# Performance work log

Hardware: AMD Instinct MI355X
Metric: run time of the kernel (lower is better)

The kernel has to match this reference:

```python
import jax, jax.numpy as jnp
import numpy as np

VOLRADIUS = 256.0
DT = 1.0 / VOLRADIUS  # self.dt = dt / volradius with dt=1.0
N_STEPS = 64
B, H, W, K, M = 1, 256, 256, 64, 16


def setup_inputs() -> dict:
    rng = np.random.default_rng(0)
    # orthographic-ish ray bundle looking down +z through the primitive cloud
    ys, xs = np.meshgrid(np.linspace(-1., 1., H, dtype=np.float32),
                         np.linspace(-1., 1., W, dtype=np.float32), indexing='ij')
    raypos = np.broadcast_to(np.stack([xs, ys, np.full_like(xs, -0.125)], -1)[None],
                             (B, H, W, 3)).astype(np.float32).copy()
    raydir = np.zeros((B, H, W, 3), np.float32); raydir[..., 2] = 1.0
    tmin = np.zeros((B, H, W), np.float32)
    tminmax = np.stack([tmin, tmin + N_STEPS * DT], -1).astype(np.float32)
    # primpos is in WORLD units (module divides by volradius)
    primpos = rng.uniform(-0.1 * VOLRADIUS, 0.1 * VOLRADIUS, (B, K, 3)).astype(np.float32)
    q, _ = np.linalg.qr(rng.normal(size=(B, K, 3, 3)))
    primrot = q.astype(np.float32)
    primscale = rng.uniform(8., 16., (B, K, 3)).astype(np.float32)  # inverse half-extent
    primrgba = rng.uniform(0., 1., (B, K, 4, M, M, M)).astype(np.float32)
    return {
        'raypos': jnp.asarray(raypos), 'raydir': jnp.asarray(raydir),
        'tminmax': jnp.asarray(tminmax), 'primpos': jnp.asarray(primpos),
        'primrot': jnp.asarray(primrot), 'primscale': jnproundtrip(primscale) if False else jnp.asarray(primscale),
        'primrgba': jnp.asarray(primrgba),
    }


def _trilinear_sum(template, pos, primpos, primrot, primscale):
    # template [K,4,M,M,M]; pos [R,3]; returns summed rgba over primitives [R,4]
    Mv = template.shape[-1]
    kidx = jnp.arange(template.shape[0])[None, :]                      # [1,K]
    rel = pos[:, None, :] - primpos[None, :, :]                        # [R,K,3]
    # local = primscale * (primrot^T @ rel), inside prim iff |local| < 1
    local = jnp.einsum('kij,rki->rkj', primrot, rel) * primscale[None]  # [R,K,3]
    inside = jnp.all(jnp.abs(local) < 1.0, axis=-1)                    # [R,K]
    g = jnp.clip((local + 1.0) * 0.5 * (Mv - 1), 0.0, Mv - 1 - 1e-5)    # voxel coords (x,y,z)
    i0 = jnp.clip(jnp.floor(g).astype(jnp.int32), 0, Mv - 2)
    f = g - i0.astype(g.dtype)
    x0, y0, z0 = i0[..., 0], i0[..., 1], i0[..., 2]
    fx, fy, fz = f[..., 0], f[..., 1], f[..., 2]
    c = jnp.zeros(local.shape[:2] + (4,), template.dtype)
    for dz, wz in ((0, 1 - fz), (1, fz)):
        for dy, wy in ((0, 1 - fy), (1, fy)):
            for dx, wx in ((0, 1 - fx), (1, fx)):
                corner = template[kidx, :, z0 + dz, y0 + dy, x0 + dx]  # [R,K,4]
                c = c + corner * (wz * wy * wx)[..., None]
    c = c * inside[..., None]
    return c.sum(axis=1)                                               # [R,4]


def _march(raypos, raydir, tminmax, primpos, primrot, primscale, template):
    Hh, Ww, _ = raypos.shape
    R = Hh * Ww
    o = raypos.reshape(R, 3)
    d = raydir.reshape(R, 3)
    tmm = tminmax.reshape(R, 2)
    tmin, tmax = tmm[:, 0], tmm[:, 1]

    def step(carry, i):
        rgb, alpha = carry
        t = tmin + (i.astype(jnp.float32) + 0.5) * DT
        valid = t < tmax
        pos = o + t[:, None] * d
        s = _trilinear_sum(template, pos, primpos, primrot, primscale)  # [R,4]
        # MVP front-to-back saturating alpha compositing (early-term equivalent)
        contrib = jnp.minimum(1.0, alpha + s[:, 3] * DT) - alpha
        contrib = jnp.where(valid, contrib, 0.0)
        rgb = rgb + s[:, :3] * contrib[:, None]
        alpha = alpha + contrib
        return (rgb, alpha), None

    init = (jnp.zeros((R, 3), jnp.float32), jnp.zeros((R,), jnp.float32))
    (rgb, alpha), _ = jax.lax.scan(jax.checkpoint(step), init, jnp.arange(N_STEPS))
    return jnp.concatenate([rgb, alpha[:, None]], -1).reshape(Hh, Ww, 4)


def reference(raypos, raydir, tminmax, primpos, primrot, primscale, primrgba):
    primpos_n = primpos / VOLRADIUS  # module normalizes primpos by volume radius
    rayrgba = jax.vmap(_march)(raypos, raydir, tminmax, primpos_n, primrot, primscale, primrgba)
    rayrgba = jnp.transpose(rayrgba, (0, 3, 1, 2))  # [B,4,H,W]
    rayrgb = rayrgba[:, :3]
    rayalpha = rayrgba[:, 3:4]
    return rayrgb, rayalpha, rayrgba
```

## Files before the change

kernel.cpp:

```cpp
#include <hip/hip_runtime.h>
#include <hip/hip_fp16.h>

#define Rtot 65536
#define Wimg 256
#define Kp 64
#define NSTEPS 64
#define DTc (1.0f/256.0f)
#define INV_VOLR (1.0f/256.0f)
#define NITEMS 16384

#define PD_OFF    0u
#define TB_OFF    4096u
#define FLAG_OFF  20480u
#define TT_OFF    65536u
#define SBUF_OFF  8388608u
#define WS_NEED   (SBUF_OFF + (size_t)NITEMS*256*8)

__device__ __forceinline__ unsigned int pack2(float a, float b) {
  __half2 h = __floats2half2_rn(a, b);
  return *(unsigned int*)&h;
}

__global__ __launch_bounds__(256) void setup_kernel(
    const float* __restrict__ raypos, const float* __restrict__ raydir,
    const float* __restrict__ tminmax, const float* __restrict__ primpos,
    const float* __restrict__ primrot, const float* __restrict__ primscale,
    const float* __restrict__ tmpl,
    float* __restrict__ tb, uint4* __restrict__ tth, float* __restrict__ pd) {
  int bid = blockIdx.x, tid = threadIdx.x;
  if (bid < 256) {
    __shared__ float smn[4][7], smx[4][7];
    int w = (bid & 15)*16 + (tid & 15);
    int h = (bid >> 4)*16 + (tid >> 4);
    int r = h*Wimg + w;
    float v[7];
    v[0] = raypos[r*3+0]; v[1] = raypos[r*3+1]; v[2] = raypos[r*3+2];
    v[3] = raydir[r*3+0]; v[4] = raydir[r*3+1]; v[5] = raydir[r*3+2];
    v[6] = tminmax[r*2+0];
    float mn[7], mx[7];
#pragma unroll
    for (int i = 0; i < 7; ++i) { mn[i] = v[i]; mx[i] = v[i]; }
#pragma unroll
    for (int m = 1; m < 64; m <<= 1) {
#pragma unroll
      for (int i = 0; i < 7; ++i) {
        mn[i] = fminf(mn[i], __shfl_xor(mn[i], m));
        mx[i] = fmaxf(mx[i], __shfl_xor(mx[i], m));
      }
    }
    int wv = tid >> 6;
    if ((tid & 63) == 0) {
#pragma unroll
      for (int i = 0; i < 7; ++i) { smn[wv][i] = mn[i]; smx[wv][i] = mx[i]; }
    }
    __syncthreads();
    if (tid == 0) {
#pragma unroll
      for (int i = 0; i < 7; ++i) {
        tb[bid*16 + i]     = fminf(fminf(smn[0][i], smn[1][i]), fminf(smn[2][i], smn[3][i]));
        tb[bid*16 + 8 + i] = fmaxf(fmaxf(smx[0][i], smx[1][i]), fmaxf(smx[2][i], smx[3][i]));
      }
    }
  } else if (bid < 320) {
    int k = bid - 256;
    const float* b0 = tmpl + (((size_t)k) << 14);
    uint4* o = tth + (k << 12);
    for (int v = tid; v < 4096; v += 256) {
      int x = v & 15;
      int xn = (x < 15) ? v + 1 : v;
      uint4 q;
      q.x = pack2(b0[v],       b0[4096+v]);
      q.y = pack2(b0[8192+v],  b0[12288+v]);
      q.z = pack2(b0[xn],      b0[4096+xn]);
      q.w = pack2(b0[8192+xn], b0[12288+xn]);
      o[v] = q;
    }
  } else {
    int k = tid;
    if (k < Kp) {
      float sc0 = primscale[k*3+0], sc1 = primscale[k*3+1], sc2 = primscale[k*3+2];
      float* o = pd + (k << 4);
      o[0] = primpos[k*3+0] * INV_VOLR;
      o[1] = primpos[k*3+1] * INV_VOLR;
      o[2] = primpos[k*3+2] * INV_VOLR;
      o[3] = 0.0f; o[4] = 0.0f; o[5] = 0.0f;
#pragma unroll
      for (int i = 0; i < 3; ++i) {
        o[6+i*3+0] = primrot[k*9+i*3+0]*sc0;
        o[6+i*3+1] = primrot[k*9+i*3+1]*sc1;
        o[6+i*3+2] = primrot[k*9+i*3+2]*sc2;
      }
      o[15] = 0.0f;
    }
  }
}

__device__ __forceinline__ void prim_setup(const float* __restrict__ p,
    float px, float py, float pz, bool& inside, const uint4*& addr,
    float& wx0, float& wfx, float& w00, float& w01, float& w10, float& w11,
    const uint4* __restrict__ tth, int k) {
  float relx = px - p[0], rely = py - p[1], relz = pz - p[2];
  float lx = relx*p[6] + rely*p[9]  + relz*p[12];
  float ly = relx*p[7] + rely*p[10] + relz*p[13];
  float lz = relx*p[8] + rely*p[11] + relz*p[14];
  inside = fabsf(lx) < 1.0f && fabsf(ly) < 1.0f && fabsf(lz) < 1.0f;
  float gx = fminf(fmaxf((lx + 1.0f)*7.5f, 0.0f), 14.99999f);
  float gy = fminf(fmaxf((ly + 1.0f)*7.5f, 0.0f), 14.99999f);
  float gz = fminf(fmaxf((lz + 1.0f)*7.5f, 0.0f), 14.99999f);
  int ix = (int)gx, iy = (int)gy, iz = (int)gz;
  ix = ix > 14 ? 14 : ix; iy = iy > 14 ? 14 : iy; iz = iz > 14 ? 14 : iz;
  float fx = gx - (float)ix, fy = gy - (float)iy, fz = gz - (float)iz;
  float m = inside ? 1.0f : 0.0f;
  wx0 = 1.0f - fx; wfx = fx;
  float wy0 = 1.0f - fy, wz0 = 1.0f - fz;
  w00 = wz0*wy0*m; w01 = wz0*fy*m; w10 = fz*wy0*m; w11 = fz*fy*m;
  addr = tth + ((size_t)k << 12) + iz*256 + iy*16 + ix;
}

#define ACCQ(q, wv, wx0, wfx) { \
  float2 p01 = __half22float2(*(const __half2*)&q.x); \
  float2 p23 = __half22float2(*(const __half2*)&q.y); \
  float2 n01 = __half22float2(*(const __half2*)&q.z); \
  float2 n23 = __half22float2(*(const __half2*)&q.w); \
  float wa = (wv)*(wx0), wb = (wv)*(wfx); \
  c0 = fmaf(p01.x, wa, fmaf(n01.x, wb, c0)); \
  c1 = fmaf(p01.y, wa, fmaf(n01.y, wb, c1)); \
  c2 = fmaf(p23.x, wa, fmaf(n23.x, wb, c2)); \
  c3 = fmaf(p23.y, wa, fmaf(n23.y, wb, c3)); }

__global__ __launch_bounds__(256) void shade_kernel(
    const float* __restrict__ raypos, const float* __restrict__ raydir,
    const float* __restrict__ tminmax, const float* __restrict__ pd,
    const float* __restrict__ tb, const uint4* __restrict__ tth,
    uint2* __restrict__ sbuf, unsigned char* __restrict__ flags) {
  __shared__ int s_list[Kp];
  __shared__ int s_cnt;
  int item = blockIdx.x;
  int tile = item >> 6, step = item & 63;
  int tid = threadIdx.x;
  if (tid < 64) {
    const float* t0 = tb + tile*16;
    float cst = ((float)step + 0.5f)*DTc;
    float tl = t0[6] + cst, th = t0[14] + cst;
    const float* p = pd + (tid << 4);
    float rlo[3], rhi[3];
#pragma unroll
    for (int a = 0; a < 3; ++a) {
      float ol = t0[a], oh = t0[8+a], dl = t0[3+a], dh = t0[11+a];
      float p1 = tl*dl, p2 = tl*dh, p3 = th*dl, p4 = th*dh;
      float lo = ol + fminf(fminf(p1, p2), fminf(p3, p4));
      float hi = oh + fmaxf(fmaxf(p1, p2), fmaxf(p3, p4));
      rlo[a] = lo - p[a];
      rhi[a] = hi - p[a];
    }
    bool pass = true;
#pragma unroll
    for (int j = 0; j < 3; ++j) {
      float llo = 0.f, lhi = 0.f;
#pragma unroll
      for (int a = 0; a < 3; ++a) {
        float rsc = p[6+a*3+j];
        float q1 = rlo[a]*rsc, q2 = rhi[a]*rsc;
        llo += fminf(q1, q2);
        lhi += fmaxf(q1, q2);
      }
      pass = pass && (llo < 1.0f) && (lhi > -1.0f);
    }
    unsigned long long mask = __ballot(pass);
    if (tid == 0) s_cnt = (int)__popcll(mask);
    if (pass) {
      int pos = (int)__popcll(mask & ((1ull << tid) - 1ull));
      s_list[pos] = tid;
    }
  }
  __syncthreads();
  int cnt = s_cnt;
  if (tid == 0) flags[item] = (unsigned char)(cnt > 0 ? 1 : 0);
  if (cnt == 0) return;

  int w = (tile & 15)*16 + (tid & 15);
  int h = (tile >> 4)*16 + (tid >> 4);
  int r = h*Wimg + w;
  float t = tminmax[r*2] + ((float)step + 0.5f)*DTc;
  float px = fmaf(t, raydir[r*3+0], raypos[r*3+0]);
  float py = fmaf(t, raydir[r*3+1], raypos[r*3+1]);
  float pz = fmaf(t, raydir[r*3+2], raypos[r*3+2]);
  float c0 = 0.f, c1 = 0.f, c2 = 0.f, c3 = 0.f;

  int j = 0;
  for (; j + 1 < cnt; j += 2) {
    int k0 = __builtin_amdgcn_readfirstlane(s_list[j]);
    int k1 = __builtin_amdgcn_readfirstlane(s_list[j+1]);
    bool in0, in1;
    const uint4 *a0, *a1;
    float wx0a, wfxa, w00a, w01a, w10a, w11a;
    float wx0b, wfxb, w00b, w01b, w10b, w11b;
    prim_setup(pd + (k0 << 4), px, py, pz, in0, a0, wx0a, wfxa, w00a, w01a, w10a, w11a, tth, k0);
    prim_setup(pd + (k1 << 4), px, py, pz, in1, a1, wx0b, wfxb, w00b, w01b, w10b, w11b, tth, k1);
    if (__any(in0 || in1)) {
      uint4 q00 = a0[0], q01 = a0[16], q10 = a0[256], q11 = a0[272];
      uint4 r00 = a1[0], r01 = a1[16], r10 = a1[256], r11 = a1[272];
      ACCQ(q00, w00a, wx0a, wfxa) ACCQ(q01, w01a, wx0a, wfxa)
      ACCQ(q10, w10a, wx0a, wfxa) ACCQ(q11, w11a, wx0a, wfxa)
      ACCQ(r00, w00b, wx0b, wfxb) ACCQ(r01, w01b, wx0b, wfxb)
      ACCQ(r10, w10b, wx0b, wfxb) ACCQ(r11, w11b, wx0b, wfxb)
    }
  }
  if (j < cnt) {
    int k0 = __builtin_amdgcn_readfirstlane(s_list[j]);
    bool in0;
    const uint4* a0;
    float wx0a, wfxa, w00a, w01a, w10a, w11a;
    prim_setup(pd + (k0 << 4), px, py, pz, in0, a0, wx0a, wfxa, w00a, w01a, w10a, w11a, tth, k0);
    if (__any(in0)) {
      uint4 q00 = a0[0], q01 = a0[16], q10 = a0[256], q11 = a0[272];
      ACCQ(q00, w00a, wx0a, wfxa) ACCQ(q01, w01a, wx0a, wfxa)
      ACCQ(q10, w10a, wx0a, wfxa) ACCQ(q11, w11a, wx0a, wfxa)
    }
  }
  sbuf[item*256 + tid] = make_uint2(pack2(c0, c1), pack2(c2, c3));
}

__global__ __launch_bounds__(256) void composite_kernel(
    const float* __restrict__ tminmax, const uint2* __restrict__ sbuf,
    const unsigned char* __restrict__ flags, float* __restrict__ out) {
  __shared__ unsigned char s_flags[NSTEPS];
  int tid = threadIdx.x;
  int b = blockIdx.x;
  if (tid < NSTEPS) s_flags[tid] = flags[b*NSTEPS + tid];
  __syncthreads();
  int w = (b & 15)*16 + (tid & 15);
  int h = (b >> 4)*16 + (tid >> 4);
  int r = h*Wimg + w;
  float tmin = tminmax[r*2+0], tmax = tminmax[r*2+1];
  float rgb0 = 0.f, rgb1 = 0.f, rgb2 = 0.f, alpha = 0.f;
  for (int i = 0; i < NSTEPS; ++i) {
    float s0 = 0.f, s1 = 0.f, s2 = 0.f, s3 = 0.f;
    if (s_flags[i]) {
      uint2 pk = sbuf[(b*NSTEPS + i)*256 + tid];
      float2 lf = __half22float2(*(__half2*)&pk.x);
      float2 hf = __half22float2(*(__half2*)&pk.y);
      s0 = lf.x; s1 = lf.y; s2 = hf.x; s3 = hf.y;
    }
    float t = tmin + ((float)i + 0.5f)*DTc;
    float contrib = fminf(1.0f, fmaf(s3, DTc, alpha)) - alpha;
    contrib = (t < tmax) ? contrib : 0.0f;
    rgb0 = fmaf(s0, contrib, rgb0);
    rgb1 = fmaf(s1, contrib, rgb1);
    rgb2 = fmaf(s2, contrib, rgb2);
    alpha += contrib;
  }
  out[0*Rtot + r] = rgb0;
  out[1*Rtot + r] = rgb1;
  out[2*Rtot + r] = rgb2;
  out[3*Rtot + r] = alpha;
  out[4*Rtot + r] = rgb0;
  out[5*Rtot + r] = rgb1;
  out[6*Rtot + r] = rgb2;
  out[7*Rtot + r] = alpha;
}

__global__ __launch_bounds__(256) void fallback_kernel(
    const float* __restrict__ raypos, const float* __restrict__ raydir,
    const float* __restrict__ tminmax,
    const float* __restrict__ primpos, const float* __restrict__ primrot,
    const float* __restrict__ primscale, const float* __restrict__ tmpl,
    float* __restrict__ out) {
  __shared__ float s_pd[Kp][16];
  int tx = threadIdx.x, ty = threadIdx.y;
  int tid = ty*16 + tx;
  if (tid < Kp) {
    int k = tid;
    float sc0 = primscale[k*3+0], sc1 = primscale[k*3+1], sc2 = primscale[k*3+2];
    s_pd[k][0] = primpos[k*3+0]*INV_VOLR;
    s_pd[k][1] = primpos[k*3+1]*INV_VOLR;
    s_pd[k][2] = primpos[k*3+2]*INV_VOLR;
#pragma unroll
    for (int i = 0; i < 3; ++i) {
      s_pd[k][6+i*3+0] = primrot[k*9+i*3+0]*sc0;
      s_pd[k][6+i*3+1] = primrot[k*9+i*3+1]*sc1;
      s_pd[k][6+i*3+2] = primrot[k*9+i*3+2]*sc2;
    }
  }
  __syncthreads();
  int w = blockIdx.x*16 + tx, h = blockIdx.y*16 + ty;
  int r = h*Wimg + w;
  float ox = raypos[r*3+0], oy = raypos[r*3+1], oz = raypos[r*3+2];
  float dx = raydir[r*3+0], dy = raydir[r*3+1], dz = raydir[r*3+2];
  float tmin = tminmax[r*2+0], tmax = tminmax[r*2+1];
  float rgb0=0.f, rgb1=0.f, rgb2=0.f, alpha=0.f;
  for (int i = 0; i < NSTEPS; ++i) {
    float t = tmin + ((float)i + 0.5f)*DTc;
    float px = fmaf(t, dx, ox), py = fmaf(t, dy, oy), pz = fmaf(t, dz, oz);
    float c[4] = {0.f, 0.f, 0.f, 0.f};
    for (int k = 0; k < Kp; ++k) {
      const float* p = &s_pd[k][0];
      float relx = px - p[0], rely = py - p[1], relz = pz - p[2];
      float lx = relx*p[6] + rely*p[9]  + relz*p[12];
      float ly = relx*p[7] + rely*p[10] + relz*p[13];
      float lz = relx*p[8] + rely*p[11] + relz*p[14];
      if (!(fabsf(lx) < 1.0f && fabsf(ly) < 1.0f && fabsf(lz) < 1.0f)) continue;
      float gx = fminf(fmaxf((lx + 1.0f)*7.5f, 0.0f), 14.99999f);
      float gy = fminf(fmaxf((ly + 1.0f)*7.5f, 0.0f), 14.99999f);
      float gz = fminf(fmaxf((lz + 1.0f)*7.5f, 0.0f), 14.99999f);
      int ix = (int)gx, iy = (int)gy, iz = (int)gz;
      ix = ix > 14 ? 14 : ix; iy = iy > 14 ? 14 : iy; iz = iz > 14 ? 14 : iz;
      float fx = gx - (float)ix, fy = gy - (float)iy, fz = gz - (float)iz;
      float wx0 = 1.0f - fx, wy0 = 1.0f - fy, wz0 = 1.0f - fz;
      float w00 = wz0*wy0, w01 = wz0*fy, w10 = fz*wy0, w11 = fz*fy;
      const float* base = tmpl + (((size_t)k) << 14) + iz*256 + iy*16 + ix;
#pragma unroll
      for (int ch = 0; ch < 4; ++ch) {
        const float* bb = base + ch*4096;
        c[ch] += (bb[0]  *wx0 + bb[1]  *fx) * w00
               + (bb[16] *wx0 + bb[17] *fx) * w01
               + (bb[256]*wx0 + bb[257]*fx) * w10
               + (bb[272]*wx0 + bb[273]*fx) * w11;
      }
    }
    float contrib = fminf(1.0f, fmaf(c[3], DTc, alpha)) - alpha;
    contrib = (t < tmax) ? contrib : 0.0f;
    rgb0 = fmaf(c[0], contrib, rgb0);
    rgb1 = fmaf(c[1], contrib, rgb1);
    rgb2 = fmaf(c[2], contrib, rgb2);
    alpha += contrib;
  }
  out[0*Rtot + r] = rgb0;
  out[1*Rtot + r] = rgb1;
  out[2*Rtot + r] = rgb2;
  out[3*Rtot + r] = alpha;
  out[4*Rtot + r] = rgb0;
  out[5*Rtot + r] = rgb1;
  out[6*Rtot + r] = rgb2;
  out[7*Rtot + r] = alpha;
}

extern "C" void kernel_launch(void* const* d_in, const int* in_sizes, int n_in,
                              void* d_out, int out_size, void* d_ws, size_t ws_size,
                              hipStream_t stream) {
  const float* raypos    = (const float*)d_in[0];
  const float* raydir    = (const float*)d_in[1];
  const float* tminmax   = (const float*)d_in[2];
  const float* primpos   = (const float*)d_in[3];
  const float* primrot   = (const float*)d_in[4];
  const float* primscale = (const float*)d_in[5];
  const float* primrgba  = (const float*)d_in[6];
  float* out = (float*)d_out;

  if (ws_size >= WS_NEED) {
    char* ws = (char*)d_ws;
    float* pd            = (float*)(ws + PD_OFF);
    float* tb            = (float*)(ws + TB_OFF);
    unsigned char* flags = (unsigned char*)(ws + FLAG_OFF);
    uint4* tth           = (uint4*)(ws + TT_OFF);
    uint2* sbuf          = (uint2*)(ws + SBUF_OFF);

    setup_kernel<<<321, 256, 0, stream>>>(raypos, raydir, tminmax, primpos,
                                          primrot, primscale, primrgba,
                                          tb, tth, pd);
    shade_kernel<<<NITEMS, 256, 0, stream>>>(raypos, raydir, tminmax, pd, tb,
                                             tth, sbuf, flags);
    composite_kernel<<<256, 256, 0, stream>>>(tminmax, sbuf, flags, out);
  } else {
    fallback_kernel<<<dim3(16,16), dim3(16,16), 0, stream>>>(
        raypos, raydir, tminmax, primpos, primrot, primscale, primrgba, out);
  }
}
```

Before: 76.61 us.

## Software-pipeline primitive gathers and use packed fp16 dot2 for trilinear accumulation

The shade kernel now issues the next primitive's setup and texture gathers before accumulating the previous one, a two-stage software pipeline that hides gather latency. The half-precision template is repacked so each word holds a channel's x0/x1 pair, which lets trilinear accumulation use fdot2 with fp16 precomputed weights instead of unpacking to float. Nontemporal loads and stores are added for ray inputs, the intermediate buffer and the outputs. Weights rounded to fp16 lose some accuracy, and the ix>14 clamp was dropped, which relies on the earlier clamp to 14.99999 to keep indices in range.

```diff
diff --git a/kernel.cpp b/kernel.cpp
--- a/kernel.cpp
+++ b/kernel.cpp
@@ -16,10 +16,24 @@
 #define SBUF_OFF  8388608u
 #define WS_NEED   (SBUF_OFF + (size_t)NITEMS*256*8)
 
+typedef _Float16 half2v __attribute__((ext_vector_type(2)));
+
+__device__ __forceinline__ half2v u2h(unsigned int u) {
+  union { unsigned int u; half2v h; } x; x.u = u; return x.h;
+}
+__device__ __forceinline__ half2v mkh2(float a, float b) {
+  half2v h; h.x = (_Float16)a; h.y = (_Float16)b; return h;
+}
 __device__ __forceinline__ unsigned int pack2(float a, float b) {
   __half2 h = __floats2half2_rn(a, b);
   return *(unsigned int*)&h;
 }
+
+#if __has_builtin(__builtin_amdgcn_fdot2)
+#define FDOT2(a, b, c) __builtin_amdgcn_fdot2((a), (b), (c), false)
+#else
+#define FDOT2(a, b, c) ((float)(a).x*(float)(b).x + (float)(a).y*(float)(b).y + (c))
+#endif
 
 __global__ __launch_bounds__(256) void setup_kernel(
     const float* __restrict__ raypos, const float* __restrict__ raydir,
@@ -69,10 +83,10 @@
       int x = v & 15;
       int xn = (x < 15) ? v + 1 : v;
       uint4 q;
-      q.x = pack2(b0[v],       b0[4096+v]);
-      q.y = pack2(b0[8192+v],  b0[12288+v]);
-      q.z = pack2(b0[xn],      b0[4096+xn]);
-      q.w = pack2(b0[8192+xn], b0[12288+xn]);
+      q.x = pack2(b0[v],         b0[xn]);
+      q.y = pack2(b0[4096+v],    b0[4096+xn]);
+      q.z = pack2(b0[8192+v],    b0[8192+xn]);
+      q.w = pack2(b0[12288+v],   b0[12288+xn]);
       o[v] = q;
     }
   } else {
@@ -95,44 +109,55 @@
   }
 }
 
-__device__ __forceinline__ void prim_setup(const float* __restrict__ p,
-    float px, float py, float pz, bool& inside, const uint4*& addr,
-    float& wx0, float& wfx, float& w00, float& w01, float& w10, float& w11,
-    const uint4* __restrict__ tth, int k) {
-  float relx = px - p[0], rely = py - p[1], relz = pz - p[2];
-  float lx = relx*p[6] + rely*p[9]  + relz*p[12];
-  float ly = relx*p[7] + rely*p[10] + relz*p[13];
-  float lz = relx*p[8] + rely*p[11] + relz*p[14];
-  inside = fabsf(lx) < 1.0f && fabsf(ly) < 1.0f && fabsf(lz) < 1.0f;
-  float gx = fminf(fmaxf((lx + 1.0f)*7.5f, 0.0f), 14.99999f);
-  float gy = fminf(fmaxf((ly + 1.0f)*7.5f, 0.0f), 14.99999f);
-  float gz = fminf(fmaxf((lz + 1.0f)*7.5f, 0.0f), 14.99999f);
-  int ix = (int)gx, iy = (int)gy, iz = (int)gz;
-  ix = ix > 14 ? 14 : ix; iy = iy > 14 ? 14 : iy; iz = iz > 14 ? 14 : iz;
-  float fx = gx - (float)ix, fy = gy - (float)iy, fz = gz - (float)iz;
-  float m = inside ? 1.0f : 0.0f;
-  wx0 = 1.0f - fx; wfx = fx;
-  float wy0 = 1.0f - fy, wz0 = 1.0f - fz;
-  w00 = wz0*wy0*m; w01 = wz0*fy*m; w10 = fz*wy0*m; w11 = fz*fy*m;
-  addr = tth + ((size_t)k << 12) + iz*256 + iy*16 + ix;
-}
-
-#define ACCQ(q, wv, wx0, wfx) { \
-  float2 p01 = __half22float2(*(const __half2*)&q.x); \
-  float2 p23 = __half22float2(*(const __half2*)&q.y); \
-  float2 n01 = __half22float2(*(const __half2*)&q.z); \
-  float2 n23 = __half22float2(*(const __half2*)&q.w); \
-  float wa = (wv)*(wx0), wb = (wv)*(wfx); \
-  c0 = fmaf(p01.x, wa, fmaf(n01.x, wb, c0)); \
-  c1 = fmaf(p01.y, wa, fmaf(n01.y, wb, c1)); \
-  c2 = fmaf(p23.x, wa, fmaf(n23.x, wb, c2)); \
-  c3 = fmaf(p23.y, wa, fmaf(n23.y, wb, c3)); }
+#define PRIM_SETUP(S, K)                                                     \
+  { const float* p = pd + ((K) << 4);                                        \
+    float relx = px - p[0], rely = py - p[1], relz = pz - p[2];              \
+    float lx = relx*p[6] + rely*p[9]  + relz*p[12];                          \
+    float ly = relx*p[7] + rely*p[10] + relz*p[13];                          \
+    float lz = relx*p[8] + rely*p[11] + relz*p[14];                          \
+    bool inside = fabsf(lx) < 1.0f && fabsf(ly) < 1.0f && fabsf(lz) < 1.0f;  \
+    any##S = __any(inside);                                                  \
+    float gx = fminf(fmaxf((lx + 1.0f)*7.5f, 0.0f), 14.99999f);              \
+    float gy = fminf(fmaxf((ly + 1.0f)*7.5f, 0.0f), 14.99999f);              \
+    float gz = fminf(fmaxf((lz + 1.0f)*7.5f, 0.0f), 14.99999f);              \
+    int ix = (int)gx, iy = (int)gy, iz = (int)gz;                            \
+    float fx = gx - (float)ix, fy = gy - (float)iy, fz = gz - (float)iz;     \
+    float m = inside ? 1.0f : 0.0f;                                          \
+    float wy0 = 1.0f - fy, wz0m = (1.0f - fz)*m, fzm = fz*m;                 \
+    float wx0 = 1.0f - fx;                                                   \
+    float w00 = wz0m*wy0, w01 = wz0m*fy, w10 = fzm*wy0, w11 = fzm*fy;        \
+    w2_0##S = mkh2(w00*wx0, w00*fx);                                         \
+    w2_1##S = mkh2(w01*wx0, w01*fx);                                         \
+    w2_2##S = mkh2(w10*wx0, w10*fx);                                         \
+    w2_3##S = mkh2(w11*wx0, w11*fx);                                         \
+    const uint4* a = tth + ((size_t)(K) << 12) + (iz*256 + iy*16 + ix);      \
+    if (any##S) { q0##S = a[0]; q1##S = a[16]; q2##S = a[256]; q3##S = a[272]; } }
+
+#define PRIM_ACC(S)                                                          \
+  if (any##S) {                                                              \
+    c0 = FDOT2(u2h(q0##S.x), w2_0##S, c0);                                   \
+    c1 = FDOT2(u2h(q0##S.y), w2_0##S, c1);                                   \
+    c2 = FDOT2(u2h(q0##S.z), w2_0##S, c2);                                   \
+    c3 = FDOT2(u2h(q0##S.w), w2_0##S, c3);                                   \
+    c0 = FDOT2(u2h(q1##S.x), w2_1##S, c0);                                   \
+    c1 = FDOT2(u2h(q1##S.y), w2_1##S, c1);                                   \
+    c2 = FDOT2(u2h(q1##S.z), w2_1##S, c2);                                   \
+    c3 = FDOT2(u2h(q1##S.w), w2_1##S, c3);                                   \
+    c0 = FDOT2(u2h(q2##S.x), w2_2##S, c0);                                   \
+    c1 = FDOT2(u2h(q2##S.y), w2_2##S, c1);                                   \
+    c2 = FDOT2(u2h(q2##S.z), w2_2##S, c2);                                   \
+    c3 = FDOT2(u2h(q2##S.w), w2_2##S, c3);                                   \
+    c0 = FDOT2(u2h(q3##S.x), w2_3##S, c0);                                   \
+    c1 = FDOT2(u2h(q3##S.y), w2_3##S, c1);                                   \
+    c2 = FDOT2(u2h(q3##S.z), w2_3##S, c2);                                   \
+    c3 = FDOT2(u2h(q3##S.w), w2_3##S, c3);                                   \
+  }
 
 __global__ __launch_bounds__(256) void shade_kernel(
     const float* __restrict__ raypos, const float* __restrict__ raydir,
     const float* __restrict__ tminmax, const float* __restrict__ pd,
     const float* __restrict__ tb, const uint4* __restrict__ tth,
-    uint2* __restrict__ sbuf, unsigned char* __restrict__ flags) {
+    unsigned long long* __restrict__ sbuf, unsigned char* __restrict__ flags) {
   __shared__ int s_list[Kp];
   __shared__ int s_cnt;
   int item = blockIdx.x;
@@ -181,48 +206,47 @@
   int w = (tile & 15)*16 + (tid & 15);
   int h = (tile >> 4)*16 + (tid >> 4);
   int r = h*Wimg + w;
-  float t = tminmax[r*2] + ((float)step + 0.5f)*DTc;
-  float px = fmaf(t, raydir[r*3+0], raypos[r*3+0]);
-  float py = fmaf(t, raydir[r*3+1], raypos[r*3+1]);
-  float pz = fmaf(t, raydir[r*3+2], raypos[r*3+2]);
+  float t = __builtin_nontemporal_load(&tminmax[r*2]) + ((float)step + 0.5f)*DTc;
+  float px = fmaf(t, __builtin_nontemporal_load(&raydir[r*3+0]),
+                     __builtin_nontemporal_load(&raypos[r*3+0]));
+  float py = fmaf(t, __builtin_nontemporal_load(&raydir[r*3+1]),
+                     __builtin_nontemporal_load(&raypos[r*3+1]));
+  float pz = fmaf(t, __builtin_nontemporal_load(&raydir[r*3+2]),
+                     __builtin_nontemporal_load(&raypos[r*3+2]));
   float c0 = 0.f, c1 = 0.f, c2 = 0.f, c3 = 0.f;
 
-  int j = 0;
-  for (; j + 1 < cnt; j += 2) {
-    int k0 = __builtin_amdgcn_readfirstlane(s_list[j]);
-    int k1 = __builtin_amdgcn_readfirstlane(s_list[j+1]);
-    bool in0, in1;
-    const uint4 *a0, *a1;
-    float wx0a, wfxa, w00a, w01a, w10a, w11a;
-    float wx0b, wfxb, w00b, w01b, w10b, w11b;
-    prim_setup(pd + (k0 << 4), px, py, pz, in0, a0, wx0a, wfxa, w00a, w01a, w10a, w11a, tth, k0);
-    prim_setup(pd + (k1 << 4), px, py, pz, in1, a1, wx0b, wfxb, w00b, w01b, w10b, w11b, tth, k1);
-    if (__any(in0 || in1)) {
-      uint4 q00 = a0[0], q01 = a0[16], q10 = a0[256], q11 = a0[272];
-      uint4 r00 = a1[0], r01 = a1[16], r10 = a1[256], r11 = a1[272];
-      ACCQ(q00, w00a, wx0a, wfxa) ACCQ(q01, w01a, wx0a, wfxa)
-      ACCQ(q10, w10a, wx0a, wfxa) ACCQ(q11, w11a, wx0a, wfxa)
-      ACCQ(r00, w00b, wx0b, wfxb) ACCQ(r01, w01b, wx0b, wfxb)
-      ACCQ(r10, w10b, wx0b, wfxb) ACCQ(r11, w11b, wx0b, wfxb)
-    }
+  bool anyA, anyB;
+  uint4 q0A, q1A, q2A, q3A, q0B, q1B, q2B, q3B;
+  half2v w2_0A, w2_1A, w2_2A, w2_3A, w2_0B, w2_1B, w2_2B, w2_3B;
+
+  int k = __builtin_amdgcn_readfirstlane(s_list[0]);
+  PRIM_SETUP(A, k)
+  int j = 1;
+  while (j + 1 < cnt) {
+    k = __builtin_amdgcn_readfirstlane(s_list[j]);
+    PRIM_SETUP(B, k)
+    PRIM_ACC(A)
+    k = __builtin_amdgcn_readfirstlane(s_list[j+1]);
+    PRIM_SETUP(A, k)
+    PRIM_ACC(B)
+    j += 2;
   }
   if (j < cnt) {
-    int k0 = __builtin_amdgcn_readfirstlane(s_list[j]);
-    bool in0;
-    const uint4* a0;
-    float wx0a, wfxa, w00a, w01a, w10a, w11a;
-    prim_setup(pd + (k0 << 4), px, py, pz, in0, a0, wx0a, wfxa, w00a, w01a, w10a, w11a, tth, k0);
-    if (__any(in0)) {
-      uint4 q00 = a0[0], q01 = a0[16], q10 = a0[256], q11 = a0[272];
-      ACCQ(q00, w00a, wx0a, wfxa) ACCQ(q01, w01a, wx0a, wfxa)
-      ACCQ(q10, w10a, wx0a, wfxa) ACCQ(q11, w11a, wx0a, wfxa)
-    }
-  }
-  sbuf[item*256 + tid] = make_uint2(pack2(c0, c1), pack2(c2, c3));
+    k = __builtin_amdgcn_readfirstlane(s_list[j]);
+    PRIM_SETUP(B, k)
+    PRIM_ACC(A)
+    PRIM_ACC(B)
+  } else {
+    PRIM_ACC(A)
+  }
+
+  unsigned long long pk = ((unsigned long long)pack2(c2, c3) << 32)
+                        | (unsigned long long)pack2(c0, c1);
+  __builtin_nontemporal_store(pk, &sbuf[item*256 + tid]);
 }
 
 __global__ __launch_bounds__(256) void composite_kernel(
-    const float* __restrict__ tminmax, const uint2* __restrict__ sbuf,
+    const float* __restrict__ tminmax, const unsigned long long* __restrict__ sbuf,
     const unsigned char* __restrict__ flags, float* __restrict__ out) {
   __shared__ unsigned char s_flags[NSTEPS];
   int tid = threadIdx.x;
@@ -237,9 +261,10 @@
   for (int i = 0; i < NSTEPS; ++i) {
     float s0 = 0.f, s1 = 0.f, s2 = 0.f, s3 = 0.f;
     if (s_flags[i]) {
-      uint2 pk = sbuf[(b*NSTEPS + i)*256 + tid];
-      float2 lf = __half22float2(*(__half2*)&pk.x);
-      float2 hf = __half22float2(*(__half2*)&pk.y);
+      unsigned long long pk = __builtin_nontemporal_load(&sbuf[(b*NSTEPS + i)*256 + tid]);
+      unsigned int lo = (unsigned int)pk, hi = (unsigned int)(pk >> 32);
+      float2 lf = __half22float2(*(__half2*)&lo);
+      float2 hf = __half22float2(*(__half2*)&hi);
       s0 = lf.x; s1 = lf.y; s2 = hf.x; s3 = hf.y;
     }
     float t = tmin + ((float)i + 0.5f)*DTc;
@@ -250,14 +275,14 @@
     rgb2 = fmaf(s2, contrib, rgb2);
     alpha += contrib;
   }
-  out[0*Rtot + r] = rgb0;
-  out[1*Rtot + r] = rgb1;
-  out[2*Rtot + r] = rgb2;
-  out[3*Rtot + r] = alpha;
-  out[4*Rtot + r] = rgb0;
-  out[5*Rtot + r] = rgb1;
-  out[6*Rtot + r] = rgb2;
-  out[7*Rtot + r] = alpha;
+  __builtin_nontemporal_store(rgb0,  &out[0*Rtot + r]);
+  __builtin_nontemporal_store(rgb1,  &out[1*Rtot + r]);
+  __builtin_nontemporal_store(rgb2,  &out[2*Rtot + r]);
+  __builtin_nontemporal_store(alpha, &out[3*Rtot + r]);
+  __builtin_nontemporal_store(rgb0,  &out[4*Rtot + r]);
+  __builtin_nontemporal_store(rgb1,  &out[5*Rtot + r]);
+  __builtin_nontemporal_store(rgb2,  &out[6*Rtot + r]);
+  __builtin_nontemporal_store(alpha, &out[7*Rtot + r]);
 }
 
 __global__ __launch_bounds__(256) void fallback_kernel(
@@ -353,7 +378,7 @@
     float* tb            = (float*)(ws + TB_OFF);
     unsigned char* flags = (unsigned char*)(ws + FLAG_OFF);
     uint4* tth           = (uint4*)(ws + TT_OFF);
-    uint2* sbuf          = (uint2*)(ws + SBUF_OFF);
+    unsigned long long* sbuf = (unsigned long long*)(ws + SBUF_OFF);
 
     setup_kernel<<<321, 256, 0, stream>>>(raypos, raydir, tminmax, primpos,
                                           primrot, primscale, primrgba,
```

New measurement: 84.02 us. +9.7%, slower.
